# Optimization experiments

Measured on AMD Instinct MI355X. Metric: run time of the kernel, lower is better.

The kernel has to match this reference:

```python
import jax, jax.numpy as jnp
import numpy as np

DIM = 33          # LUT lattice size per color axis
B, H, W = 4, 2048, 2048


def setup_inputs() -> dict:
    key = jax.random.key(0)
    k1, k2 = jax.random.split(key)
    # pixel values in [0, 1) index the LUT lattice
    x = jax.random.uniform(k1, (B, 3, H, W), dtype=jnp.float32)
    # module initializes LUT to zeros; use small random values so the
    # interpolation (and its gradient) is non-trivial for testing
    LUT = 0.1 * jax.random.normal(k2, (3, DIM, DIM, DIM), dtype=jnp.float32)
    return {"x": x, "LUT": LUT}


def _trilinear_lut(LUT, x):
    """Trilinear 3D LUT interpolation (image-adaptive-3DLUT trilinear op).

    LUT: (3, D, D, D) indexed as LUT[c, b_idx, g_idx, r_idx]
    x:   (B, 3, H, W) RGB in [0, 1]
    returns (B, 3, H, W)
    """
    D = LUT.shape[1]
    bins = D - 1  # number of cells per axis (binsize = 1/bins)
    rr = x[:, 0] * bins  # (B, H, W) continuous lattice coords
    gg = x[:, 1] * bins
    bb = x[:, 2] * bins
    r0 = jnp.clip(jnp.floor(rr).astype(jnp.int32), 0, bins - 1)
    g0 = jnp.clip(jnp.floor(gg).astype(jnp.int32), 0, bins - 1)
    b0 = jnp.clip(jnp.floor(bb).astype(jnp.int32), 0, bins - 1)
    fr = rr - r0  # fractional offsets within the cell
    fg = gg - g0
    fb = bb - b0

    acc = jnp.zeros((3,) + r0.shape, dtype=LUT.dtype)  # (3, B, H, W)
    for db in (0, 1):
        wb = fb if db else (1.0 - fb)
        for dg in (0, 1):
            wg = fg if dg else (1.0 - fg)
            for dr in (0, 1):
                wr = fr if dr else (1.0 - fr)
                w = (wb * wg * wr)[None]                     # (1, B, H, W)
                acc = acc + w * LUT[:, b0 + db, g0 + dg, r0 + dr]
    return jnp.transpose(acc, (1, 0, 2, 3))  # (B, 3, H, W)


def reference(x, LUT):
    return _trilinear_lut(LUT, x)
```

## Files before the change

### kernel.cpp

```cpp
#include <hip/hip_runtime.h>

#define DIMK 33
#define D2   (DIMK * DIMK)
#define D3   (DIMK * DIMK * DIMK)
#define NVPAD 35940
#define HWPIX (2048 * 2048)
#define HWSHIFT 22

typedef float        f32x4 __attribute__((ext_vector_type(4)));
typedef unsigned int u32;
typedef u32          u32x4 __attribute__((ext_vector_type(4)));

#define QTAB_OFF_BYTES 256

__global__ __launch_bounds__(256) void k_absmax(const float* __restrict__ LUT,
                                                u32* __restrict__ ws) {
    int t = blockIdx.x * 256 + threadIdx.x;
    float m = 0.0f;
    for (int i = t; i < 3 * D3; i += (int)gridDim.x * 256)
        m = fmaxf(m, fabsf(LUT[i]));
    for (int off = 32; off; off >>= 1)
        m = fmaxf(m, __shfl_down(m, off, 64));
    if ((threadIdx.x & 63) == 0)
        atomicMax(ws, __float_as_uint(m));
}

__global__ __launch_bounds__(256) void k_quant(const float* __restrict__ LUT,
                                               const u32* __restrict__ ws,
                                               u32* __restrict__ qtab) {
    int t = blockIdx.x * 256 + threadIdx.x;
    if (t >= D3) return;
    float s = __uint_as_float(*ws);
    s = fmaxf(s, 1e-20f);
    float inv = 511.0f / s;
    u32 w = 0;
#pragma unroll
    for (int c = 0; c < 3; ++c) {
        float v = LUT[c * D3 + t];
        int q = (int)rintf(v * inv);
        q = max(-511, min(511, q));
        w |= ((u32)(q + 512)) << (10 * c);
    }
    qtab[t] = w;
}

__global__ __launch_bounds__(1024, 4) void k_apply(const float* __restrict__ x,
                                                   const u32* __restrict__ qtab,
                                                   const u32* __restrict__ ws,
                                                   float* __restrict__ out,
                                                   int nquads) {
    __shared__ u32 tab[NVPAD];

    const int stride = (int)gridDim.x * 1024;
    int t = blockIdx.x * 1024 + threadIdx.x;

    f32x4 r4 = {0.f, 0.f, 0.f, 0.f}, g4 = r4, b4 = r4;
    if (t < nquads) {
        int p = t << 2;
        int b = p >> HWSHIFT;
        int o = p & (HWPIX - 1);
        const float* xb = x + (size_t)b * 3 * HWPIX + o;
        r4 = __builtin_nontemporal_load((const f32x4*)(xb));
        g4 = __builtin_nontemporal_load((const f32x4*)(xb + HWPIX));
        b4 = __builtin_nontemporal_load((const f32x4*)(xb + 2 * HWPIX));
    }

    {
        u32x4* dst = (u32x4*)tab;
        const u32x4* src = (const u32x4*)qtab;
        for (int i = threadIdx.x; i < NVPAD / 4; i += 1024)
            dst[i] = src[i];
    }
    float s511 = __uint_as_float(*ws) * (1.0f / 511.0f);
    float bias = 512.0f * s511;
    __syncthreads();

    while (t < nquads) {
        int tn = t + stride;
        f32x4 nr = {0.f, 0.f, 0.f, 0.f}, ng = nr, nb = nr;
        if (tn < nquads) {
            int pn = tn << 2;
            int bn = pn >> HWSHIFT;
            int on = pn & (HWPIX - 1);
            const float* xbn = x + (size_t)bn * 3 * HWPIX + on;
            nr = __builtin_nontemporal_load((const f32x4*)(xbn));
            ng = __builtin_nontemporal_load((const f32x4*)(xbn + HWPIX));
            nb = __builtin_nontemporal_load((const f32x4*)(xbn + 2 * HWPIX));
        }

        int  vid[4];
        float fr[4], fg[4], fb[4];
#pragma unroll
        for (int i = 0; i < 4; ++i) {
            float cr = r4[i] * 32.0f;
            float cg = g4[i] * 32.0f;
            float cb = b4[i] * 32.0f;
            int ri = max(0, min(31, (int)cr));
            int gi = max(0, min(31, (int)cg));
            int bi = max(0, min(31, (int)cb));
            fr[i] = cr - (float)ri;
            fg[i] = cg - (float)gi;
            fb[i] = cb - (float)bi;
            vid[i] = bi * D2 + gi * DIMK + ri;
        }

        u32 cw[4][8];
#pragma unroll
        for (int i = 0; i < 4; ++i) {
            int v = vid[i];
            cw[i][0] = tab[v];
            cw[i][1] = tab[v + 1];
            cw[i][2] = tab[v + DIMK];
            cw[i][3] = tab[v + DIMK + 1];
            cw[i][4] = tab[v + D2];
            cw[i][5] = tab[v + D2 + 1];
            cw[i][6] = tab[v + D2 + DIMK];
            cw[i][7] = tab[v + D2 + DIMK + 1];
        }

        f32x4 oc0, oc1, oc2;
#pragma unroll
        for (int i = 0; i < 4; ++i) {
            float wr0 = 1.0f - fr[i], wg0 = 1.0f - fg[i], wb0 = 1.0f - fb[i];
            float wbg00 = wb0 * wg0, wbg01 = wb0 * fg[i];
            float wbg10 = fb[i] * wg0, wbg11 = fb[i] * fg[i];
            float w[8] = {wbg00 * wr0, wbg00 * fr[i], wbg01 * wr0, wbg01 * fr[i],
                          wbg10 * wr0, wbg10 * fr[i], wbg11 * wr0, wbg11 * fr[i]};
            float A0 = 0.f, A1 = 0.f, A2 = 0.f;
#pragma unroll
            for (int cn = 0; cn < 8; ++cn) {
                u32 c = cw[i][cn];
                A0 += w[cn] * (float)(c & 1023u);
                A1 += w[cn] * (float)((c >> 10) & 1023u);
                A2 += w[cn] * (float)((c >> 20) & 1023u);
            }
            oc0[i] = A0 * s511 - bias;
            oc1[i] = A1 * s511 - bias;
            oc2[i] = A2 * s511 - bias;
        }

        {
            int p = t << 2;
            int b = p >> HWSHIFT;
            int o = p & (HWPIX - 1);
            float* ob = out + (size_t)b * 3 * HWPIX + o;
            *(f32x4*)(ob) = oc0;
            *(f32x4*)(ob + HWPIX) = oc1;
            *(f32x4*)(ob + 2 * HWPIX) = oc2;
        }

        t = tn;
        r4 = nr;
        g4 = ng;
        b4 = nb;
    }
}

__global__ __launch_bounds__(256) void lut_apply_direct(const float* __restrict__ x,
                                                        const float* __restrict__ LUT,
                                                        float* __restrict__ out,
                                                        int nquads) {
    int t = blockIdx.x * blockDim.x + threadIdx.x;
    if (t >= nquads) return;
    int p = t << 2;
    int b = p >> HWSHIFT;
    int o = p & (HWPIX - 1);
    const float* xb = x + (size_t)b * 3 * HWPIX + o;

    f32x4 r4 = *(const f32x4*)(xb);
    f32x4 g4 = *(const f32x4*)(xb + HWPIX);
    f32x4 b4 = *(const f32x4*)(xb + 2 * HWPIX);
    f32x4 oc0, oc1, oc2;

#pragma unroll
    for (int i = 0; i < 4; ++i) {
        float fr = r4[i] * 32.0f;
        float fg = g4[i] * 32.0f;
        float fb = b4[i] * 32.0f;
        int ri = max(0, min(31, (int)fr));
        int gi = max(0, min(31, (int)fg));
        int bi = max(0, min(31, (int)fb));
        fr -= (float)ri;
        fg -= (float)gi;
        fb -= (float)bi;

        float wr1[2] = {1.0f - fr, fr};
        float wg1[2] = {1.0f - fg, fg};
        float wb1[2] = {1.0f - fb, fb};
        float a0 = 0.f, a1 = 0.f, a2 = 0.f;
#pragma unroll
        for (int db = 0; db < 2; ++db)
#pragma unroll
            for (int dg = 0; dg < 2; ++dg)
#pragma unroll
                for (int dr = 0; dr < 2; ++dr) {
                    float w = wb1[db] * wg1[dg] * wr1[dr];
                    int idx = (bi + db) * D2 + (gi + dg) * DIMK + (ri + dr);
                    a0 += w * LUT[idx];
                    a1 += w * LUT[D3 + idx];
                    a2 += w * LUT[2 * D3 + idx];
                }
        oc0[i] = a0;
        oc1[i] = a1;
        oc2[i] = a2;
    }
    float* ob = out + (size_t)b * 3 * HWPIX + o;
    *(f32x4*)(ob) = oc0;
    *(f32x4*)(ob + HWPIX) = oc1;
    *(f32x4*)(ob + 2 * HWPIX) = oc2;
}

extern "C" void kernel_launch(void* const* d_in, const int* in_sizes, int n_in,
                              void* d_out, int out_size, void* d_ws, size_t ws_size,
                              hipStream_t stream) {
    const float* x   = (const float*)d_in[0];
    const float* LUT = (const float*)d_in[1];
    float* out = (float*)d_out;

    int npix   = in_sizes[0] / 3;
    int nquads = npix >> 2;

    const size_t need = QTAB_OFF_BYTES + (size_t)NVPAD * 4;
    if (ws_size >= need) {
        u32* scale = (u32*)d_ws;
        u32* qtab  = (u32*)((char*)d_ws + QTAB_OFF_BYTES);
        hipMemsetAsync(scale, 0, 4, stream);
        k_absmax<<<128, 256, 0, stream>>>(LUT, scale);
        k_quant<<<(D3 + 255) / 256, 256, 0, stream>>>(LUT, scale, qtab);
        k_apply<<<1024, 1024, 0, stream>>>(x, qtab, scale, out, nquads);
    } else {
        int blocks = (nquads + 255) / 256;
        lut_apply_direct<<<blocks, 256, 0, stream>>>(x, LUT, out, nquads);
    }
}
```

Baseline: 350.9 us.

## Fuse LUT absmax and quantization into the apply kernel, drop extra launches

Replaces the separate memset, absmax, quantize and apply kernels with one kernel where each block computes the LUT absmax via a block reduction, quantizes the LUT into shared memory, then runs the persistent interpolation loop. The grid shrinks to 256 blocks. This removes several kernel launches and the global round trip of the packed table, but every block now redundantly reads the full float LUT twice and does the quantization work itself. The workspace-free fallback path is removed.

```diff
diff --git a/kernel.cpp b/kernel.cpp
--- a/kernel.cpp
+++ b/kernel.cpp
@@ -3,56 +3,22 @@
 #define DIMK 33
 #define D2   (DIMK * DIMK)
 #define D3   (DIMK * DIMK * DIMK)
-#define NVPAD 35940
 #define HWPIX (2048 * 2048)
 #define HWSHIFT 22
 
 typedef float        f32x4 __attribute__((ext_vector_type(4)));
 typedef unsigned int u32;
-typedef u32          u32x4 __attribute__((ext_vector_type(4)));
 
-#define QTAB_OFF_BYTES 256
+__global__ __launch_bounds__(1024, 4) void k_lut(const float* __restrict__ x,
+                                                 const float* __restrict__ LUT,
+                                                 float* __restrict__ out,
+                                                 int nquads) {
+    __shared__ u32   tab[D3];
+    __shared__ float red[16];
 
-__global__ __launch_bounds__(256) void k_absmax(const float* __restrict__ LUT,
-                                                u32* __restrict__ ws) {
-    int t = blockIdx.x * 256 + threadIdx.x;
-    float m = 0.0f;
-    for (int i = t; i < 3 * D3; i += (int)gridDim.x * 256)
-        m = fmaxf(m, fabsf(LUT[i]));
-    for (int off = 32; off; off >>= 1)
-        m = fmaxf(m, __shfl_down(m, off, 64));
-    if ((threadIdx.x & 63) == 0)
-        atomicMax(ws, __float_as_uint(m));
-}
-
-__global__ __launch_bounds__(256) void k_quant(const float* __restrict__ LUT,
-                                               const u32* __restrict__ ws,
-                                               u32* __restrict__ qtab) {
-    int t = blockIdx.x * 256 + threadIdx.x;
-    if (t >= D3) return;
-    float s = __uint_as_float(*ws);
-    s = fmaxf(s, 1e-20f);
-    float inv = 511.0f / s;
-    u32 w = 0;
-#pragma unroll
-    for (int c = 0; c < 3; ++c) {
-        float v = LUT[c * D3 + t];
-        int q = (int)rintf(v * inv);
-        q = max(-511, min(511, q));
-        w |= ((u32)(q + 512)) << (10 * c);
-    }
-    qtab[t] = w;
-}
-
-__global__ __launch_bounds__(1024, 4) void k_apply(const float* __restrict__ x,
-                                                   const u32* __restrict__ qtab,
-                                                   const u32* __restrict__ ws,
-                                                   float* __restrict__ out,
-                                                   int nquads) {
-    __shared__ u32 tab[NVPAD];
-
+    const int tid    = threadIdx.x;
     const int stride = (int)gridDim.x * 1024;
-    int t = blockIdx.x * 1024 + threadIdx.x;
+    int t = blockIdx.x * 1024 + tid;
 
     f32x4 r4 = {0.f, 0.f, 0.f, 0.f}, g4 = r4, b4 = r4;
     if (t < nquads) {
@@ -65,14 +31,45 @@
         b4 = __builtin_nontemporal_load((const f32x4*)(xb + 2 * HWPIX));
     }
 
+    float m = 0.0f;
     {
-        u32x4* dst = (u32x4*)tab;
-        const u32x4* src = (const u32x4*)qtab;
-        for (int i = threadIdx.x; i < NVPAD / 4; i += 1024)
-            dst[i] = src[i];
+        const int n4 = (3 * D3) >> 2;
+        const f32x4* L4 = (const f32x4*)LUT;
+        for (int i = tid; i < n4; i += 1024) {
+            f32x4 v = L4[i];
+            m = fmaxf(m, fmaxf(fmaxf(fabsf(v.x), fabsf(v.y)),
+                               fmaxf(fabsf(v.z), fabsf(v.w))));
+        }
+        for (int i = (n4 << 2) + tid; i < 3 * D3; i += 1024)
+            m = fmaxf(m, fabsf(LUT[i]));
     }
-    float s511 = __uint_as_float(*ws) * (1.0f / 511.0f);
-    float bias = 512.0f * s511;
+    for (int off = 32; off; off >>= 1)
+        m = fmaxf(m, __shfl_down(m, off, 64));
+    if ((tid & 63) == 0) red[tid >> 6] = m;
+    __syncthreads();
+    if (tid == 0) {
+        float mm = red[0];
+#pragma unroll
+        for (int i = 1; i < 16; ++i) mm = fmaxf(mm, red[i]);
+        red[0] = fmaxf(mm, 1e-20f);
+    }
+    __syncthreads();
+    const float s    = red[0];
+    const float inv  = 511.0f / s;
+    const float s511 = s * (1.0f / 511.0f);
+    const float bias = 512.0f * s511;
+
+    for (int v = tid; v < D3; v += 1024) {
+        u32 w = 0;
+#pragma unroll
+        for (int c = 0; c < 3; ++c) {
+            float vv = LUT[c * D3 + v];
+            int q = (int)rintf(vv * inv);
+            q = max(-511, min(511, q));
+            w |= ((u32)(q + 512)) << (10 * c);
+        }
+        tab[v] = w;
+    }
     __syncthreads();
 
     while (t < nquads) {
@@ -88,7 +85,7 @@
             nb = __builtin_nontemporal_load((const f32x4*)(xbn + 2 * HWPIX));
         }
 
-        int  vid[4];
+        int   vid[4];
         float fr[4], fg[4], fb[4];
 #pragma unroll
         for (int i = 0; i < 4; ++i) {
@@ -122,7 +119,7 @@
 #pragma unroll
         for (int i = 0; i < 4; ++i) {
             float wr0 = 1.0f - fr[i], wg0 = 1.0f - fg[i], wb0 = 1.0f - fb[i];
-            float wbg00 = wb0 * wg0, wbg01 = wb0 * fg[i];
+            float wbg00 = wb0 * wg0,   wbg01 = wb0 * fg[i];
             float wbg10 = fb[i] * wg0, wbg11 = fb[i] * fg[i];
             float w[8] = {wbg00 * wr0, wbg00 * fr[i], wbg01 * wr0, wbg01 * fr[i],
                           wbg10 * wr0, wbg10 * fr[i], wbg11 * wr0, wbg11 * fr[i]};
@@ -144,70 +141,16 @@
             int b = p >> HWSHIFT;
             int o = p & (HWPIX - 1);
             float* ob = out + (size_t)b * 3 * HWPIX + o;
-            *(f32x4*)(ob) = oc0;
-            *(f32x4*)(ob + HWPIX) = oc1;
+            *(f32x4*)(ob)             = oc0;
+            *(f32x4*)(ob + HWPIX)     = oc1;
             *(f32x4*)(ob + 2 * HWPIX) = oc2;
         }
 
-        t = tn;
+        t  = tn;
         r4 = nr;
         g4 = ng;
         b4 = nb;
     }
-}
-
-__global__ __launch_bounds__(256) void lut_apply_direct(const float* __restrict__ x,
-                                                        const float* __restrict__ LUT,
-                                                        float* __restrict__ out,
-                                                        int nquads) {
-    int t = blockIdx.x * blockDim.x + threadIdx.x;
-    if (t >= nquads) return;
-    int p = t << 2;
-    int b = p >> HWSHIFT;
-    int o = p & (HWPIX - 1);
-    const float* xb = x + (size_t)b * 3 * HWPIX + o;
-
-    f32x4 r4 = *(const f32x4*)(xb);
-    f32x4 g4 = *(const f32x4*)(xb + HWPIX);
-    f32x4 b4 = *(const f32x4*)(xb + 2 * HWPIX);
-    f32x4 oc0, oc1, oc2;
-
-#pragma unroll
-    for (int i = 0; i < 4; ++i) {
-        float fr = r4[i] * 32.0f;
-        float fg = g4[i] * 32.0f;
-        float fb = b4[i] * 32.0f;
-        int ri = max(0, min(31, (int)fr));
-        int gi = max(0, min(31, (int)fg));
-        int bi = max(0, min(31, (int)fb));
-        fr -= (float)ri;
-        fg -= (float)gi;
-        fb -= (float)bi;
-
-        float wr1[2] = {1.0f - fr, fr};
-        float wg1[2] = {1.0f - fg, fg};
-        float wb1[2] = {1.0f - fb, fb};
-        float a0 = 0.f, a1 = 0.f, a2 = 0.f;
-#pragma unroll
-        for (int db = 0; db < 2; ++db)
-#pragma unroll
-            for (int dg = 0; dg < 2; ++dg)
-#pragma unroll
-                for (int dr = 0; dr < 2; ++dr) {
-                    float w = wb1[db] * wg1[dg] * wr1[dr];
-                    int idx = (bi + db) * D2 + (gi + dg) * DIMK + (ri + dr);
-                    a0 += w * LUT[idx];
-                    a1 += w * LUT[D3 + idx];
-                    a2 += w * LUT[2 * D3 + idx];
-                }
-        oc0[i] = a0;
-        oc1[i] = a1;
-        oc2[i] = a2;
-    }
-    float* ob = out + (size_t)b * 3 * HWPIX + o;
-    *(f32x4*)(ob) = oc0;
-    *(f32x4*)(ob + HWPIX) = oc1;
-    *(f32x4*)(ob + 2 * HWPIX) = oc2;
 }
 
 extern "C" void kernel_launch(void* const* d_in, const int* in_sizes, int n_in,
@@ -220,16 +163,5 @@
     int npix   = in_sizes[0] / 3;
     int nquads = npix >> 2;
 
-    const size_t need = QTAB_OFF_BYTES + (size_t)NVPAD * 4;
-    if (ws_size >= need) {
-        u32* scale = (u32*)d_ws;
-        u32* qtab  = (u32*)((char*)d_ws + QTAB_OFF_BYTES);
-        hipMemsetAsync(scale, 0, 4, stream);
-        k_absmax<<<128, 256, 0, stream>>>(LUT, scale);
-        k_quant<<<(D3 + 255) / 256, 256, 0, stream>>>(LUT, scale, qtab);
-        k_apply<<<1024, 1024, 0, stream>>>(x, qtab, scale, out, nquads);
-    } else {
-        int blocks = (nquads + 255) / 256;
-        lut_apply_direct<<<blocks, 256, 0, stream>>>(x, LUT, out, nquads);
-    }
+    k_lut<<<256, 1024, 0, stream>>>(x, LUT, out, nquads);
 }
```

Measured after the change: 350.6 us. About the same (-0.1%).
